# Performance work log

Hardware: AMD Instinct MI355X
Metric: run time of the kernel (lower is better)

Reference implementation:

```python
import jax, jax.numpy as jnp
import numpy as np

DIM = 2                 # spatial dimension (fixed to 2 in the source)
T = 6                   # number_of_time_points
DT = 1.0 / (T - 1)


def _mlp(z, W1, b1, W2, b2, W3, b3):
    # Linear_Tanh(4->10), Linear_Tanh(10->10), Linear(10->3)
    h = jnp.tanh(z @ W1 + b1)
    h = jnp.tanh(h @ W2 + b2)
    return h @ W3 + b3


def _sym_block(o):
    # o[...,3] -> symmetric 2x2 block: off-diag o[...,0], diag exp(o[...,1]), exp(o[...,2])
    off = o[..., 0]
    row0 = jnp.stack([jnp.exp(o[..., 1]), off], axis=-1)
    row1 = jnp.stack([off, jnp.exp(o[..., 2])], axis=-1)
    return jnp.stack([row0, row1], axis=-2)


def _kernel_blocks(x, y, params):
    # x: [b, nx, 2], y: [b, ny, 2] -> pairwise 2x2 kernel blocks [b, nx, ny, 2, 2]
    b, nx, _ = x.shape
    ny = y.shape[1]
    xx = jnp.broadcast_to(x[:, :, None, :], (b, nx, ny, DIM))
    yy = jnp.broadcast_to(y[:, None, :, :], (b, nx, ny, DIM))
    K1 = _sym_block(_mlp(jnp.concatenate([xx, yy], axis=-1), *params))
    K2 = _sym_block(_mlp(jnp.concatenate([yy, xx], axis=-1), *params))
    return 0.5 * (K1 + K2)


def _matvec(K, q):
    # block-matrix vector product: K [b,nx,ny,2,2] @ q [b,ny,2] -> [b,nx,2]
    return jnp.einsum('bxyij,byj->bxi', K, q)


def _forward(q_0, template_points, control_points, W1, b1, W2, b2, W3, b3):
    params = (W1, b1, W2, b2, W3, b3)
    bts = q_0.shape[0]
    p = jnp.broadcast_to(control_points[None], (bts,) + control_points.shape)
    p_t, q_t = [p], [q_0]

    def ham(pp, qq):
        dh_dq = _matvec(_kernel_blocks(pp, pp, params), qq)
        return 0.5 * jnp.sum(qq * dh_dq), dh_dq

    # Hamiltonian shooting: T steps of symplectic-Euler-like integration
    for _ in range(T):
        pc, qc = p_t[-1], q_t[-1]
        (_, dh_dq), dh_dp = jax.value_and_grad(ham, has_aux=True)(pc, qc)
        p_t.append(pc + DT * dh_dq)
        q_t.append(qc - DT * dh_dp)

    # flow the template points along the time-varying velocity field
    x = jnp.broadcast_to(template_points[None], (bts,) + template_points.shape)
    for pc, qc in zip(p_t, q_t):
        x = x + DT * _matvec(_kernel_blocks(x, pc, params), qc)
    return x


def setup_inputs() -> dict:
    key = jax.random.key(0)
    ks = jax.random.split(key, 8)
    bts, ncp, ntpl, H = 16, 64, 2048, 10
    # 8x8 control-point grid over [-2.5, 2.5]^2 (compute_grid with margin 0)
    ax = jnp.linspace(-2.5, 2.5, 8, dtype=jnp.float32)
    gx, gy = jnp.meshgrid(ax, ax, indexing='ij')
    control_points = jnp.stack([gx, gy], axis=-1).reshape(ncp, DIM)
    template_points = jax.random.normal(ks[0], (ntpl, DIM), dtype=jnp.float32)
    q_0 = 0.05 * jax.random.normal(ks[1], (bts, ncp, DIM), dtype=jnp.float32)
    W1 = 0.5 * jax.random.normal(ks[2], (2 * DIM, H), dtype=jnp.float32)
    b1 = jnp.zeros((H,), dtype=jnp.float32)
    W2 = 0.5 * jax.random.normal(ks[3], (H, H), dtype=jnp.float32)
    b2 = jnp.zeros((H,), dtype=jnp.float32)
    W3 = 0.5 * jax.random.normal(ks[4], (H, DIM * (DIM + 1) // 2), dtype=jnp.float32)
    b3 = jnp.zeros((DIM * (DIM + 1) // 2,), dtype=jnp.float32)
    return {'q_0': q_0, 'template_points': template_points, 'control_points': control_points,
            'W1': W1, 'b1': b1, 'W2': W2, 'b2': b2, 'W3': W3, 'b3': b3}


def reference(q_0, template_points, control_points, W1, b1, W2, b2, W3, b3):
    return _forward(q_0, template_points, control_points, W1, b1, W2, b2, W3, b3)
```

## Files before the change

kernel.cpp:

```cpp
#include <hip/hip_runtime.h>

#define NCP    64
#define BTS    16
#define NTPL   2048
#define TSTEPS 6
#define DTF    0.2f
#define L2E    1.4426950408889634f

__device__ __forceinline__ float fast_rcp(float x) { return __builtin_amdgcn_rcpf(x); }
__device__ __forceinline__ float fexp2(float x)    { return __builtin_amdgcn_exp2f(x); }
__device__ __forceinline__ float fast_tanh(float x) {
    float e = __expf(2.0f * x);
    return 1.0f - 2.0f * fast_rcp(1.0f + e);
}

__device__ __forceinline__ void kblock(
    float x0, float x1, float p0, float p1,
    const float (&w)[180], float b2t_0_, const float* __restrict__ wt,
    float& M00, float& M01, float& M11)
{
    float ra[10], rb[10];
#pragma unroll
    for (int k = 0; k < 10; ++k) {
        float ta = fmaf(p1, w[30 + k],
                   fmaf(p0, w[20 + k],
                   fmaf(x1, w[10 + k],
                   fmaf(x0, w[k], w[40 + k]))));
        float tb = fmaf(x1, w[30 + k],
                   fmaf(x0, w[20 + k],
                   fmaf(p1, w[10 + k],
                   fmaf(p0, w[k], w[40 + k]))));
        ra[k] = fast_rcp(1.0f + fexp2(ta));
        rb[k] = fast_rcp(1.0f + fexp2(tb));
    }
    float ua[10], ub[10];
#pragma unroll
    for (int k = 0; k < 10; ++k) {
        float bb = wt[150 + k];
        ua[k] = fmaf(ra[0], w[50 + k], bb);
        ub[k] = fmaf(rb[0], w[50 + k], bb);
    }
#pragma unroll
    for (int c = 1; c < 10; ++c) {
#pragma unroll
        for (int k = 0; k < 10; ++k) {
            float ww = w[50 + c * 10 + k];
            ua[k] = fmaf(ra[c], ww, ua[k]);
            ub[k] = fmaf(rb[c], ww, ub[k]);
        }
    }
    float Oa = wt[190], Ob = wt[190];
    float T1a = wt[191], T1b = wt[191];
    float T2a = wt[192], T2b = wt[192];
#pragma unroll
    for (int c = 0; c < 10; ++c) {
        float r2a = fast_rcp(1.0f + fexp2(ua[c]));
        float r2b = fast_rcp(1.0f + fexp2(ub[c]));
        Oa  = fmaf(r2a, w[150 + c], Oa);   Ob  = fmaf(r2b, w[150 + c], Ob);
        T1a = fmaf(r2a, w[160 + c], T1a);  T1b = fmaf(r2b, w[160 + c], T1b);
        T2a = fmaf(r2a, w[170 + c], T2a);  T2b = fmaf(r2b, w[170 + c], T2b);
    }
    M00 = fexp2(T1a) + fexp2(T1b);
    M01 = Oa + Ob;
    M11 = fexp2(T2a) + fexp2(T2b);
    (void)b2t_0_;
}

__device__ __forceinline__ void load_w(const float* __restrict__ wt,
                                       int lane, float (&w)[180])
{
    float c0 = wt[lane];
    float c1 = wt[64 + lane];
    float c2 = wt[128 + lane];
#pragma unroll
    for (int t = 0; t < 180; ++t) {
        int src = (t < 150) ? t : (t + 10);
        int ch = src >> 6, ix = src & 63;
        float v = (ch == 0) ? c0 : (ch == 1) ? c1 : c2;
        w[t] = __shfl(v, ix);
    }
}

__global__ __launch_bounds__(64, 1)
void shoot_step(const float* __restrict__ q0, const float* __restrict__ cp,
                const float* __restrict__ p_in, const float* __restrict__ q_in,
                float* __restrict__ p_out, float* __restrict__ q_out,
                const float* __restrict__ W1, const float* __restrict__ b1,
                const float* __restrict__ W2, const float* __restrict__ b2,
                const float* __restrict__ W3, const float* __restrict__ b3,
                float* __restrict__ wt, int first)
{
    int blk = blockIdx.x;
    if (first && blk == BTS * NCP) {
        int t = threadIdx.x;
        if (t < 40) wt[t] = 2.0f * L2E * W1[t];
        if (t < 10) wt[40 + t] = 2.0f * L2E * b1[t];
        for (int i = t; i < 100; i += 64) wt[50 + i] = -4.0f * L2E * W2[i];
        if (t < 10) {
            float s = b2[t];
            for (int c = 0; c < 10; ++c) s += W2[c * 10 + t];
            wt[150 + t] = 2.0f * L2E * s;
            wt[160 + t] = -W3[t * 3 + 0];
            wt[170 + t] = -2.0f * L2E * W3[t * 3 + 1];
            wt[180 + t] = -2.0f * L2E * W3[t * 3 + 2];
        }
        if (t < 3) {
            float s = b3[t];
            for (int c = 0; c < 10; ++c) s += W3[c * 3 + t];
            wt[190 + t] = (t == 0) ? 0.5f * s : fmaf(L2E, s, -1.0f);
        }
        return;
    }

    int batch = blk >> 6;
    int a = blk & (NCP - 1);
    int b = threadIdx.x;

    float pax, pay, qax, qay, pbx, pby, qbx, qby;
    if (first) {
        pax = cp[2 * a]; pay = cp[2 * a + 1];
        pbx = cp[2 * b]; pby = cp[2 * b + 1];
        qax = q0[(batch * NCP + a) * 2 + 0]; qay = q0[(batch * NCP + a) * 2 + 1];
        qbx = q0[(batch * NCP + b) * 2 + 0]; qby = q0[(batch * NCP + b) * 2 + 1];
    } else {
        const float* pB = p_in + batch * NCP * 2;
        const float* qB = q_in + batch * NCP * 2;
        pax = pB[a * 2 + 0]; pay = pB[a * 2 + 1];
        qax = qB[a * 2 + 0]; qay = qB[a * 2 + 1];
        pbx = pB[b * 2 + 0]; pby = pB[b * 2 + 1];
        qbx = qB[b * 2 + 0]; qby = qB[b * 2 + 1];
    }

    float dhq_x = 0.f, dhq_y = 0.f;
    float g_x = 0.f, g_y = 0.f;
    float cross = fmaf(qax, qby, qay * qbx);

#pragma unroll
    for (int e = 0; e < 2; ++e) {
        float z0 = e ? pbx : pax;
        float z1 = e ? pby : pay;
        float z2 = e ? pax : pbx;
        float z3 = e ? pay : pby;

        float h1[10];
#pragma unroll
        for (int k = 0; k < 10; ++k) {
            float u = fmaf(z3, W1[30 + k],
                      fmaf(z2, W1[20 + k],
                      fmaf(z1, W1[10 + k],
                      fmaf(z0, W1[k], b1[k]))));
            h1[k] = fast_tanh(u);
        }
        float u2[10];
#pragma unroll
        for (int k = 0; k < 10; ++k) u2[k] = b2[k];
#pragma unroll
        for (int c = 0; c < 10; ++c) {
#pragma unroll
            for (int k = 0; k < 10; ++k) u2[k] = fmaf(h1[c], W2[c * 10 + k], u2[k]);
        }
        float h2[10];
        float o0 = b3[0], o1 = b3[1], o2 = b3[2];
#pragma unroll
        for (int c = 0; c < 10; ++c) {
            h2[c] = fast_tanh(u2[c]);
            o0 = fmaf(h2[c], W3[c * 3 + 0], o0);
            o1 = fmaf(h2[c], W3[c * 3 + 1], o1);
            o2 = fmaf(h2[c], W3[c * 3 + 2], o2);
        }
        float e1 = __expf(o1), e2 = __expf(o2);

        dhq_x = fmaf(0.5f, fmaf(e1, qbx, o0 * qby), dhq_x);
        dhq_y = fmaf(0.5f, fmaf(o0, qbx, e2 * qby), dhq_y);

        float d0 = cross;
        float d1 = e1 * qax * qbx;
        float d2 = e2 * qay * qby;

        float du2[10];
#pragma unroll
        for (int c = 0; c < 10; ++c) {
            float dh2 = fmaf(W3[c * 3 + 0], d0,
                        fmaf(W3[c * 3 + 1], d1, W3[c * 3 + 2] * d2));
            du2[c] = dh2 * (1.0f - h2[c] * h2[c]);
        }
        float du1[10];
#pragma unroll
        for (int c = 0; c < 10; ++c) {
            float dh1 = 0.f;
#pragma unroll
            for (int k = 0; k < 10; ++k) dh1 = fmaf(W2[c * 10 + k], du2[k], dh1);
            du1[c] = dh1 * (1.0f - h1[c] * h1[c]);
        }
        int c0 = e ? 2 : 0;
        float ga = 0.f, gb = 0.f;
#pragma unroll
        for (int k = 0; k < 10; ++k) {
            ga = fmaf(W1[(0 + c0) * 10 + k], du1[k], ga);
            gb = fmaf(W1[(1 + c0) * 10 + k], du1[k], gb);
        }
        g_x = fmaf(0.5f, ga, g_x);
        g_y = fmaf(0.5f, gb, g_y);
    }

#pragma unroll
    for (int off = 32; off > 0; off >>= 1) {
        dhq_x += __shfl_xor(dhq_x, off);
        dhq_y += __shfl_xor(dhq_y, off);
        g_x   += __shfl_xor(g_x, off);
        g_y   += __shfl_xor(g_y, off);
    }

    if (b == 0) {
        float* pO = p_out + (batch * NCP + a) * 2;
        float* qO = q_out + (batch * NCP + a) * 2;
        pO[0] = fmaf(DTF, dhq_x, pax);
        pO[1] = fmaf(DTF, dhq_y, pay);
        qO[0] = fmaf(-DTF, g_x, qax);
        qO[1] = fmaf(-DTF, g_y, qay);
    }
}

__global__ __launch_bounds__(256, 1)
void flow_step0(const float* __restrict__ tpl, const float* __restrict__ cp,
                const float* __restrict__ q0, float* __restrict__ out,
                const float* __restrict__ wt)
{
    int i = blockIdx.x * 4 + (threadIdx.x >> 6);
    int j = threadIdx.x & 63;

    float w[180];
    load_w(wt, j, w);

    float x0 = tpl[2 * i], x1 = tpl[2 * i + 1];
    float p0 = cp[2 * j],  p1 = cp[2 * j + 1];

    float M00, M01, M11;
    kblock(x0, x1, p0, p1, w, 0.f, wt, M00, M01, M11);

    const float2* __restrict__ q = (const float2*)q0;
#pragma unroll
    for (int bt = 0; bt < BTS; ++bt) {
        float2 qq = q[bt * NCP + j];
        float vx = fmaf(M00, qq.x, M01 * qq.y);
        float vy = fmaf(M01, qq.x, M11 * qq.y);
#pragma unroll
        for (int off = 32; off > 0; off >>= 1) {
            vx += __shfl_xor(vx, off);
            vy += __shfl_xor(vy, off);
        }
        if (j == 0) {
            out[((size_t)bt * NTPL + i) * 2 + 0] = fmaf(DTF, vx, x0);
            out[((size_t)bt * NTPL + i) * 2 + 1] = fmaf(DTF, vy, x1);
        }
    }
}

__global__ __launch_bounds__(256, 1)
void flow_rest(const float* __restrict__ p_hist, const float* __restrict__ q_hist,
               float* __restrict__ out, const float* __restrict__ wt)
{
    int unit = blockIdx.x * 4 + (threadIdx.x >> 6);
    int j = threadIdx.x & 63;
    int batch = unit >> 11;
    int i = unit & (NTPL - 1);

    float w[180];
    load_w(wt, j, w);

    const float2* __restrict__ ph = (const float2*)p_hist;
    const float2* __restrict__ qh = (const float2*)q_hist;

    size_t oidx = ((size_t)batch * NTPL + i) * 2;
    float x0 = out[oidx + 0];
    float x1 = out[oidx + 1];

#pragma unroll
    for (int s = 0; s < TSTEPS; ++s) {
        int idx = ((s + 1) * BTS + batch) * NCP + j;
        float2 P = ph[idx];
        float2 Q = qh[idx];
        float M00, M01, M11;
        kblock(x0, x1, P.x, P.y, w, 0.f, wt, M00, M01, M11);
        float vx = fmaf(M00, Q.x, M01 * Q.y);
        float vy = fmaf(M01, Q.x, M11 * Q.y);
#pragma unroll
        for (int off = 32; off > 0; off >>= 1) {
            vx += __shfl_xor(vx, off);
            vy += __shfl_xor(vy, off);
        }
        x0 = fmaf(DTF, vx, x0);
        x1 = fmaf(DTF, vy, x1);
    }

    if (j == 0) {
        out[oidx + 0] = x0;
        out[oidx + 1] = x1;
    }
}

extern "C" void kernel_launch(void* const* d_in, const int* in_sizes, int n_in,
                              void* d_out, int out_size, void* d_ws, size_t ws_size,
                              hipStream_t stream)
{
    const float* q0  = (const float*)d_in[0];
    const float* tpl = (const float*)d_in[1];
    const float* cp  = (const float*)d_in[2];
    const float* W1  = (const float*)d_in[3];
    const float* b1  = (const float*)d_in[4];
    const float* W2  = (const float*)d_in[5];
    const float* b2  = (const float*)d_in[6];
    const float* W3  = (const float*)d_in[7];
    const float* b3  = (const float*)d_in[8];
    float* out = (float*)d_out;

    float* ws = (float*)d_ws;
    const int slab = BTS * NCP * 2;
    float* p_hist = ws;
    float* q_hist = ws + (size_t)7 * slab;
    float* wt     = ws + (size_t)14 * slab;

    shoot_step<<<BTS * NCP + 1, 64, 0, stream>>>(
        q0, cp, nullptr, nullptr,
        p_hist + (size_t)1 * slab, q_hist + (size_t)1 * slab,
        W1, b1, W2, b2, W3, b3, wt, 1);
    for (int s = 1; s < TSTEPS; ++s) {
        shoot_step<<<BTS * NCP, 64, 0, stream>>>(
            q0, cp,
            p_hist + (size_t)s * slab, q_hist + (size_t)s * slab,
            p_hist + (size_t)(s + 1) * slab, q_hist + (size_t)(s + 1) * slab,
            W1, b1, W2, b2, W3, b3, wt, 0);
    }

    flow_step0<<<NTPL / 4, 256, 0, stream>>>(tpl, cp, q0, out, wt);
    flow_rest<<<BTS * NTPL / 4, 256, 0, stream>>>(p_hist, q_hist, out, wt);
}
```

Measured before the change: 320.1 us.

## Batch sigmoid reciprocals four at a time and launch flow kernels as single-wave blocks

```diff
diff --git a/kernel.cpp b/kernel.cpp
--- a/kernel.cpp
+++ b/kernel.cpp
@@ -14,24 +14,45 @@
     return 1.0f - 2.0f * fast_rcp(1.0f + e);
 }
 
+__device__ __forceinline__ void sig4(float t0, float t1, float t2, float t3,
+                                     float& r0, float& r1, float& r2, float& r3)
+{
+    float d0 = 1.0f + fexp2(t0);
+    float d1 = 1.0f + fexp2(t1);
+    float d2 = 1.0f + fexp2(t2);
+    float d3 = 1.0f + fexp2(t3);
+    float p01 = d0 * d1, p23 = d2 * d3;
+    float inv = fast_rcp(p01 * p23);
+    float i01 = inv * p23, i23 = inv * p01;
+    r0 = d1 * i01;  r1 = d0 * i01;
+    r2 = d3 * i23;  r3 = d2 * i23;
+}
+
 __device__ __forceinline__ void kblock(
     float x0, float x1, float p0, float p1,
-    const float (&w)[180], float b2t_0_, const float* __restrict__ wt,
+    const float (&w)[180], const float* __restrict__ wt,
     float& M00, float& M01, float& M11)
 {
     float ra[10], rb[10];
 #pragma unroll
-    for (int k = 0; k < 10; ++k) {
-        float ta = fmaf(p1, w[30 + k],
-                   fmaf(p0, w[20 + k],
-                   fmaf(x1, w[10 + k],
-                   fmaf(x0, w[k], w[40 + k]))));
-        float tb = fmaf(x1, w[30 + k],
-                   fmaf(x0, w[20 + k],
-                   fmaf(p1, w[10 + k],
-                   fmaf(p0, w[k], w[40 + k]))));
-        ra[k] = fast_rcp(1.0f + fexp2(ta));
-        rb[k] = fast_rcp(1.0f + fexp2(tb));
+    for (int k = 0; k < 10; k += 2) {
+        float ta0 = fmaf(p1, w[30 + k],
+                    fmaf(p0, w[20 + k],
+                    fmaf(x1, w[10 + k],
+                    fmaf(x0, w[k], w[40 + k]))));
+        float tb0 = fmaf(x1, w[30 + k],
+                    fmaf(x0, w[20 + k],
+                    fmaf(p1, w[10 + k],
+                    fmaf(p0, w[k], w[40 + k]))));
+        float ta1 = fmaf(p1, w[31 + k],
+                    fmaf(p0, w[21 + k],
+                    fmaf(x1, w[11 + k],
+                    fmaf(x0, w[k + 1], w[41 + k]))));
+        float tb1 = fmaf(x1, w[31 + k],
+                    fmaf(x0, w[21 + k],
+                    fmaf(p1, w[11 + k],
+                    fmaf(p0, w[k + 1], w[41 + k]))));
+        sig4(ta0, tb0, ta1, tb1, ra[k], rb[k], ra[k + 1], rb[k + 1]);
     }
     float ua[10], ub[10];
 #pragma unroll
@@ -53,17 +74,19 @@
     float T1a = wt[191], T1b = wt[191];
     float T2a = wt[192], T2b = wt[192];
 #pragma unroll
-    for (int c = 0; c < 10; ++c) {
-        float r2a = fast_rcp(1.0f + fexp2(ua[c]));
-        float r2b = fast_rcp(1.0f + fexp2(ub[c]));
-        Oa  = fmaf(r2a, w[150 + c], Oa);   Ob  = fmaf(r2b, w[150 + c], Ob);
-        T1a = fmaf(r2a, w[160 + c], T1a);  T1b = fmaf(r2b, w[160 + c], T1b);
-        T2a = fmaf(r2a, w[170 + c], T2a);  T2b = fmaf(r2b, w[170 + c], T2b);
+    for (int c = 0; c < 10; c += 2) {
+        float g0a, g0b, g1a, g1b;
+        sig4(ua[c], ub[c], ua[c + 1], ub[c + 1], g0a, g0b, g1a, g1b);
+        Oa  = fmaf(g0a, w[150 + c], Oa);   Ob  = fmaf(g0b, w[150 + c], Ob);
+        T1a = fmaf(g0a, w[160 + c], T1a);  T1b = fmaf(g0b, w[160 + c], T1b);
+        T2a = fmaf(g0a, w[170 + c], T2a);  T2b = fmaf(g0b, w[170 + c], T2b);
+        Oa  = fmaf(g1a, w[151 + c], Oa);   Ob  = fmaf(g1b, w[151 + c], Ob);
+        T1a = fmaf(g1a, w[161 + c], T1a);  T1b = fmaf(g1b, w[161 + c], T1b);
+        T2a = fmaf(g1a, w[171 + c], T2a);  T2b = fmaf(g1b, w[171 + c], T2b);
     }
     M00 = fexp2(T1a) + fexp2(T1b);
     M01 = Oa + Ob;
     M11 = fexp2(T2a) + fexp2(T2b);
-    (void)b2t_0_;
 }
 
 __device__ __forceinline__ void load_w(const float* __restrict__ wt,
@@ -221,13 +244,13 @@
     }
 }
 
-__global__ __launch_bounds__(256, 1)
+__global__ __launch_bounds__(64, 4)
 void flow_step0(const float* __restrict__ tpl, const float* __restrict__ cp,
                 const float* __restrict__ q0, float* __restrict__ out,
                 const float* __restrict__ wt)
 {
-    int i = blockIdx.x * 4 + (threadIdx.x >> 6);
-    int j = threadIdx.x & 63;
+    int i = blockIdx.x;
+    int j = threadIdx.x;
 
     float w[180];
     load_w(wt, j, w);
@@ -236,7 +259,7 @@
     float p0 = cp[2 * j],  p1 = cp[2 * j + 1];
 
     float M00, M01, M11;
-    kblock(x0, x1, p0, p1, w, 0.f, wt, M00, M01, M11);
+    kblock(x0, x1, p0, p1, w, wt, M00, M01, M11);
 
     const float2* __restrict__ q = (const float2*)q0;
 #pragma unroll
@@ -256,12 +279,12 @@
     }
 }
 
-__global__ __launch_bounds__(256, 1)
+__global__ __launch_bounds__(64, 4)
 void flow_rest(const float* __restrict__ p_hist, const float* __restrict__ q_hist,
                float* __restrict__ out, const float* __restrict__ wt)
 {
-    int unit = blockIdx.x * 4 + (threadIdx.x >> 6);
-    int j = threadIdx.x & 63;
+    int unit = blockIdx.x;
+    int j = threadIdx.x;
     int batch = unit >> 11;
     int i = unit & (NTPL - 1);
 
@@ -281,7 +304,7 @@
         float2 P = ph[idx];
         float2 Q = qh[idx];
         float M00, M01, M11;
-        kblock(x0, x1, P.x, P.y, w, 0.f, wt, M00, M01, M11);
+        kblock(x0, x1, P.x, P.y, w, wt, M00, M01, M11);
         float vx = fmaf(M00, Q.x, M01 * Q.y);
         float vy = fmaf(M01, Q.x, M11 * Q.y);
 #pragma unroll
@@ -332,6 +355,6 @@
             W1, b1, W2, b2, W3, b3, wt, 0);
     }
 
-    flow_step0<<<NTPL / 4, 256, 0, stream>>>(tpl, cp, q0, out, wt);
-    flow_rest<<<BTS * NTPL / 4, 256, 0, stream>>>(p_hist, q_hist, out, wt);
-}
+    flow_step0<<<NTPL, 64, 0, stream>>>(tpl, cp, q0, out, wt);
+    flow_rest<<<BTS * NTPL, 64, 0, stream>>>(p_hist, q_hist, out, wt);
+}
```

After: 1.153 ms. 3.6x slower.
